# Optimization experiments

Hardware: AMD Instinct MI355X
Metric: run time of the kernel (lower is better)

## Reference

```python
import jax, jax.numpy as jnp
import numpy as np

N_NODES = 100000


def _gcn_conv(x, W, b, row, col, norm, n_nodes):
    # PyG GCNConv: h = x @ W; out[i] = sum_{(j->i)} norm_e * h[j] + b
    h = x @ W
    msg = h[row] * norm[:, None]              # [E_tot, out_dim] gather
    out = jax.ops.segment_sum(msg, col, num_segments=n_nodes)  # scatter-add
    return out + b


def _norm_and_loops(edge_index, n_nodes):
    # add self loops, compute symmetric normalization deg^-1/2 * deg^-1/2
    loop = jnp.arange(n_nodes, dtype=edge_index.dtype)
    row = jnp.concatenate([edge_index[0], loop])
    col = jnp.concatenate([edge_index[1], loop])
    deg = jax.ops.segment_sum(jnp.ones_like(col, dtype=jnp.float32), col,
                              num_segments=n_nodes)
    dis = jnp.where(deg > 0, jax.lax.rsqrt(jnp.maximum(deg, 1.0)), 0.0)
    norm = dis[row] * dis[col]
    return row, col, norm


def setup_inputs() -> dict:
    key = jax.random.key(0)
    ks = jax.random.split(key, 9)
    in_c, hid, lat = 128, 128, 64
    n_edges = 1600000
    x = jax.random.normal(ks[0], (N_NODES, in_c), dtype=jnp.float32)
    edge_index = jax.random.randint(ks[1], (2, n_edges), 0, N_NODES, dtype=jnp.int64)
    s1 = 1.0 / np.sqrt(in_c)
    s2 = 1.0 / np.sqrt(hid)
    W1 = jax.random.uniform(ks[2], (in_c, hid), jnp.float32, -s1, s1)
    b1 = jnp.zeros((hid,), jnp.float32)
    W_mu = jax.random.uniform(ks[3], (hid, lat), jnp.float32, -s2, s2)
    b_mu = jnp.zeros((lat,), jnp.float32)
    W_lv = jax.random.uniform(ks[4], (hid, lat), jnp.float32, -s2, s2)
    b_lv = jnp.zeros((lat,), jnp.float32)
    eps = jax.random.normal(ks[5], (N_NODES, lat), dtype=jnp.float32)
    return {"x": x, "edge_index": edge_index, "W1": W1, "b1": b1,
            "W_mu": W_mu, "b_mu": b_mu, "W_lv": W_lv, "b_lv": b_lv,
            "eps": eps}


def reference(x, edge_index, W1, b1, W_mu, b_mu, W_lv, b_lv, eps):
    row, col, norm = _norm_and_loops(edge_index, N_NODES)
    h = jax.nn.relu(_gcn_conv(x, W1, b1, row, col, norm, N_NODES))
    mu = _gcn_conv(h, W_mu, b_mu, row, col, norm, N_NODES)
    logvar = _gcn_conv(h, W_lv, b_lv, row, col, norm, N_NODES)
    # reparameterize (training mode): z = mu + eps * exp(0.5*logvar)
    z = mu + eps * jnp.exp(0.5 * logvar)
    return (z, mu, logvar)
```

## Files before the change

kernel.cpp:

```cpp
#include <hip/hip_runtime.h>
#include <math.h>


#define SHIFT 9
#define EPB 2048
#define HEPB 8192
#define CAP 15104

using f32x4 = __attribute__((ext_vector_type(4))) float;
using f16x8 = __attribute__((ext_vector_type(8))) _Float16;
using f16x2 = __attribute__((ext_vector_type(2))) _Float16;

__device__ inline int scan256(int v, int* wsum) {
    __syncthreads();
    int lane = threadIdx.x & 63, wid = threadIdx.x >> 6;
    int s = v;
#pragma unroll
    for (int d = 1; d < 64; d <<= 1) {
        int u = __shfl_up(s, d, 64);
        if (lane >= d) s += u;
    }
    if (lane == 63) wsum[wid] = s;
    __syncthreads();
    int off = 0;
    for (int w = 0; w < wid; w++) off += wsum[w];
    return off + s - v;
}

__global__ __launch_bounds__(256) void k_bhist(const int* __restrict__ coli,
                                               int* __restrict__ gbh,
                                               int E, int NB) {
    __shared__ int lh[4][256];
    int t = threadIdx.x, w = t >> 6;
    lh[0][t] = 0; lh[1][t] = 0; lh[2][t] = 0; lh[3][t] = 0;
    __syncthreads();
    int base = blockIdx.x * HEPB;
    for (int i = t; i < HEPB; i += 256) {
        int e = base + i;
        if (e < E) atomicAdd(&lh[w][coli[e] >> SHIFT], 1);
    }
    __syncthreads();
    if (t < NB) {
        int v = lh[0][t] + lh[1][t] + lh[2][t] + lh[3][t];
        if (v) atomicAdd(&gbh[t], v);
    }
}

__global__ __launch_bounds__(256) void k_bscan(const int* __restrict__ gbh,
                                               int* __restrict__ bptr,
                                               int* __restrict__ bcur,
                                               int NB, int E,
                                               int* __restrict__ rowptr, int N) {
    __shared__ int wsum[4];
    int t = threadIdx.x;
    int v = (t < NB) ? gbh[t] : 0;
    int e = scan256(v, wsum);
    if (t < NB) { bptr[t] = e; bcur[t] = e; }
    if (t == 0) { bptr[NB] = E; rowptr[N] = E; }
}

__global__ __launch_bounds__(256) void k_bucket(const int* __restrict__ rowi,
                                                const int* __restrict__ coli,
                                                int* __restrict__ bcur,
                                                int2* __restrict__ recs,
                                                int E, int NB) {
    __shared__ int lh[4][256], lcur[4][256], excl[256], gbase[256], wsum[4];
    __shared__ int2 stage[EPB];
    int t = threadIdx.x, w = t >> 6;
    lh[0][t] = 0; lh[1][t] = 0; lh[2][t] = 0; lh[3][t] = 0;
    __syncthreads();
    int base = blockIdx.x * EPB;
    int nE = min(EPB, E - base);
    for (int i = t; i < nE; i += 256)
        atomicAdd(&lh[w][coli[base + i] >> SHIFT], 1);
    __syncthreads();
    int h0 = lh[0][t], h1 = lh[1][t], h2 = lh[2][t], h3 = lh[3][t];
    int tot = h0 + h1 + h2 + h3;
    int ex = scan256(tot, wsum);
    excl[t] = ex;
    lcur[0][t] = ex;
    lcur[1][t] = ex + h0;
    lcur[2][t] = ex + h0 + h1;
    lcur[3][t] = ex + h0 + h1 + h2;
    if (t < NB && tot) gbase[t] = atomicAdd(&bcur[t], tot);
    __syncthreads();
    for (int i = t; i < nE; i += 256) {
        int r = rowi[base + i], c = coli[base + i];
        int p = atomicAdd(&lcur[w][c >> SHIFT], 1);
        stage[p] = make_int2(r, c);
    }
    __syncthreads();
    for (int i = t; i < nE; i += 256) {
        int2 r = stage[i];
        int bb = r.y >> SHIFT;
        recs[gbase[bb] + (i - excl[bb])] = r;
    }
}

__global__ __launch_bounds__(256) void k_fill2(const int2* __restrict__ recs,
                                               const int* __restrict__ bptr,
                                               int* __restrict__ rowptr,
                                               float* __restrict__ dis,
                                               int* __restrict__ srcs, int N) {
    __shared__ int hist[512], excl[512], wsum[4];
    __shared__ int srcsL[CAP];
    int t = threadIdx.x;
    int b = blockIdx.x;
    int nbase = b << SHIFT;
    int start = bptr[b], end = bptr[b + 1];
    int cnt = end - start;
    hist[t] = 0;
    hist[t + 256] = 0;
    __syncthreads();
    for (int i = start + t; i < end; i += 256)
        atomicAdd(&hist[recs[i].y - nbase], 1);
    __syncthreads();
    int h0 = hist[2 * t], h1 = hist[2 * t + 1];
    int e0 = scan256(h0 + h1, wsum);
    excl[2 * t] = e0;
    excl[2 * t + 1] = e0 + h0;
    int n0 = nbase + 2 * t, n1 = nbase + 2 * t + 1;
    if (n0 < N) { rowptr[n0] = start + e0;      dis[n0] = rsqrtf((float)(h0 + 1)); }
    if (n1 < N) { rowptr[n1] = start + e0 + h0; dis[n1] = rsqrtf((float)(h1 + 1)); }
    __syncthreads();
    if (cnt <= CAP) {
        for (int i = start + t; i < end; i += 256) {
            int2 r = recs[i];
            int p = atomicAdd(&excl[r.y - nbase], 1);
            srcsL[p] = r.x;
        }
        __syncthreads();
        for (int i = t; i < cnt; i += 256) srcs[start + i] = srcsL[i];
    } else {
        for (int i = start + t; i < end; i += 256) {
            int2 r = recs[i];
            int p = atomicAdd(&excl[r.y - nbase], 1);
            srcs[start + p] = r.x;
        }
    }
}

template <bool XF16>
__global__ __launch_bounds__(256) void k_gemm(const void* __restrict__ Xv,
                                              const float* __restrict__ Wa,
                                              const float* __restrict__ Wb,
                                              int split,
                                              const float* __restrict__ dis,
                                              _Float16* __restrict__ Y,
                                              int M, int ngroups) {
    __shared__ _Float16 Wl[16384];
    int tid = threadIdx.x;
    int wbs = 128 - split;
    for (int i = tid; i < 16384; i += 256) {
        int k = i >> 7, n = i & 127;
        float v = (n < split) ? Wa[k * split + n] : Wb[k * wbs + (n - split)];
        int tt = n >> 4, c = (k >> 5), q = (k >> 3) & 3, ln = q * 16 + (n & 15);
        Wl[(((tt * 4 + c) * 64) + ln) * 8 + (k & 7)] = (_Float16)v;
    }
    __syncthreads();

    int lane = tid & 63, w = tid >> 6;
    f16x8 B[32];
#pragma unroll
    for (int i = 0; i < 32; i++)
        B[i] = *(const f16x8*)&Wl[(i * 64 + lane) * 8];

    int m16 = lane & 15, quad = lane >> 4;
    for (int g = blockIdx.x; g < ngroups; g += gridDim.x) {
        int rowbase = g * 64 + w * 16;
        if (rowbase >= M) continue;
        int arow = min(rowbase + m16, M - 1);
        f16x8 A[4];
        if (XF16) {
            const _Float16* X = (const _Float16*)Xv;
#pragma unroll
            for (int c = 0; c < 4; c++)
                A[c] = *(const f16x8*)&X[arow * 128 + c * 32 + quad * 8];
        } else {
            const float* X = (const float*)Xv;
#pragma unroll
            for (int c = 0; c < 4; c++) {
                float4 u0 = *(const float4*)&X[arow * 128 + c * 32 + quad * 8];
                float4 u1 = *(const float4*)&X[arow * 128 + c * 32 + quad * 8 + 4];
                f16x8 a;
                a[0] = (_Float16)u0.x; a[1] = (_Float16)u0.y;
                a[2] = (_Float16)u0.z; a[3] = (_Float16)u0.w;
                a[4] = (_Float16)u1.x; a[5] = (_Float16)u1.y;
                a[6] = (_Float16)u1.z; a[7] = (_Float16)u1.w;
                A[c] = a;
            }
        }

        f32x4 acc[8];
#pragma unroll
        for (int t = 0; t < 8; t++) acc[t] = (f32x4)(0.f);
#pragma unroll
        for (int t = 0; t < 8; t++)
#pragma unroll
            for (int c = 0; c < 4; c++)
                acc[t] = __builtin_amdgcn_mfma_f32_16x16x32_f16(
                    A[c], B[t * 4 + c], acc[t], 0, 0, 0);

#pragma unroll
        for (int r = 0; r < 4; r++) {
            int row = rowbase + quad * 4 + r;
            if (row < M) {
                float d = dis[row];
#pragma unroll
                for (int t = 0; t < 8; t++)
                    Y[row * 128 + t * 16 + m16] = (_Float16)(d * acc[t][r]);
            }
        }
    }
}

template <bool OF16>
__global__ __launch_bounds__(256) void k_agg(const _Float16* __restrict__ F,
                                             const float* __restrict__ dis,
                                             const int* __restrict__ rowptr,
                                             const int* __restrict__ srcs,
                                             const float* __restrict__ ba,
                                             const float* __restrict__ bb,
                                             void* __restrict__ outA,
                                             void* __restrict__ outB,
                                             const float* __restrict__ eps,
                                             float* __restrict__ z, int N) {
    int node = blockIdx.x * 4 + (threadIdx.x >> 6);
    if (node >= N) return;
    int lane = threadIdx.x & 63;
    int g = lane >> 4, sl = lane & 15;
    const f16x8* Fr = (const f16x8*)F;

    float acc[8];
#pragma unroll
    for (int j = 0; j < 8; j++) acc[j] = 0.f;
    if (g == 0) {
        f16x8 v = Fr[node * 16 + sl];
#pragma unroll
        for (int j = 0; j < 8; j++) acc[j] = (float)v[j];
    }

    int s = rowptr[node], e = rowptr[node + 1];
    int t = s;
    for (; t + 8 <= e; t += 8) {
        int i0 = srcs[t + g];
        int i1 = srcs[t + 4 + g];
        f16x8 v0 = Fr[i0 * 16 + sl];
        f16x8 v1 = Fr[i1 * 16 + sl];
#pragma unroll
        for (int j = 0; j < 8; j++)
            acc[j] += (float)v0[j] + (float)v1[j];
    }
    if (t + 4 <= e) {
        int i0 = srcs[t + g];
        f16x8 v0 = Fr[i0 * 16 + sl];
#pragma unroll
        for (int j = 0; j < 8; j++) acc[j] += (float)v0[j];
        t += 4;
    }
    if (t < e) {
        int idx = t + g;
        bool ok = idx < e;
        int i0 = ok ? srcs[idx] : 0;
        f16x8 v0 = Fr[i0 * 16 + sl];
        if (ok) {
#pragma unroll
            for (int j = 0; j < 8; j++) acc[j] += (float)v0[j];
        }
    }

#pragma unroll
    for (int j = 0; j < 8; j++) {
        acc[j] += __shfl_xor(acc[j], 16);
        acc[j] += __shfl_xor(acc[j], 32);
    }

    float di = dis[node];
    if constexpr (OF16) {
        float4 b0 = *(const float4*)&ba[sl * 8];
        float4 b1 = *(const float4*)&ba[sl * 8 + 4];
        if (lane < 16) {
            f16x8 o;
            o[0] = (_Float16)fmaxf(fmaf(di, acc[0], b0.x), 0.f);
            o[1] = (_Float16)fmaxf(fmaf(di, acc[1], b0.y), 0.f);
            o[2] = (_Float16)fmaxf(fmaf(di, acc[2], b0.z), 0.f);
            o[3] = (_Float16)fmaxf(fmaf(di, acc[3], b0.w), 0.f);
            o[4] = (_Float16)fmaxf(fmaf(di, acc[4], b1.x), 0.f);
            o[5] = (_Float16)fmaxf(fmaf(di, acc[5], b1.y), 0.f);
            o[6] = (_Float16)fmaxf(fmaf(di, acc[6], b1.z), 0.f);
            o[7] = (_Float16)fmaxf(fmaf(di, acc[7], b1.w), 0.f);
            ((f16x8*)outA)[node * 16 + sl] = o;
        }
    } else {
        const float* bp = (sl < 8) ? ba : bb;
        int cb = (sl & 7) * 8;
        float4 b0 = *(const float4*)&bp[cb];
        float4 b1 = *(const float4*)&bp[cb + 4];
        float o[8];
        o[0] = fmaf(di, acc[0], b0.x);
        o[1] = fmaf(di, acc[1], b0.y);
        o[2] = fmaf(di, acc[2], b0.z);
        o[3] = fmaf(di, acc[3], b0.w);
        o[4] = fmaf(di, acc[4], b1.x);
        o[5] = fmaf(di, acc[5], b1.y);
        o[6] = fmaf(di, acc[6], b1.z);
        o[7] = fmaf(di, acc[7], b1.w);
        if (lane < 16) {
            float* op = (sl < 8) ? (float*)outA : (float*)outB;
            f32x4 s0, s1;
            s0[0] = o[0]; s0[1] = o[1]; s0[2] = o[2]; s0[3] = o[3];
            s1[0] = o[4]; s1[1] = o[5]; s1[2] = o[6]; s1[3] = o[7];
            __builtin_nontemporal_store(s0, (f32x4*)&op[node * 64 + cb]);
            __builtin_nontemporal_store(s1, (f32x4*)&op[node * 64 + cb + 4]);
        }
        float lvv[8];
#pragma unroll
        for (int j = 0; j < 8; j++) lvv[j] = __shfl_xor(o[j], 8);
        if (lane < 8) {
            int zb = node * 64 + sl * 8;
            float4 e0 = *(const float4*)&eps[zb];
            float4 e1 = *(const float4*)&eps[zb + 4];
            f32x4 z0, z1;
            z0[0] = fmaf(e0.x, expf(0.5f * lvv[0]), o[0]);
            z0[1] = fmaf(e0.y, expf(0.5f * lvv[1]), o[1]);
            z0[2] = fmaf(e0.z, expf(0.5f * lvv[2]), o[2]);
            z0[3] = fmaf(e0.w, expf(0.5f * lvv[3]), o[3]);
            z1[0] = fmaf(e1.x, expf(0.5f * lvv[4]), o[4]);
            z1[1] = fmaf(e1.y, expf(0.5f * lvv[5]), o[5]);
            z1[2] = fmaf(e1.z, expf(0.5f * lvv[6]), o[6]);
            z1[3] = fmaf(e1.w, expf(0.5f * lvv[7]), o[7]);
            __builtin_nontemporal_store(z0, (f32x4*)&z[zb]);
            __builtin_nontemporal_store(z1, (f32x4*)&z[zb + 4]);
        }
    }
}

extern "C" void kernel_launch(void* const* d_in, const int* in_sizes, int n_in,
                              void* d_out, int out_size, void* d_ws, size_t ws_size,
                              hipStream_t stream) {
    const float* x   = (const float*)d_in[0];
    const int*   ei  = (const int*)d_in[1];
    const float* W1  = (const float*)d_in[2];
    const float* b1  = (const float*)d_in[3];
    const float* Wmu = (const float*)d_in[4];
    const float* bmu = (const float*)d_in[5];
    const float* Wlv = (const float*)d_in[6];
    const float* blv = (const float*)d_in[7];
    const float* eps = (const float*)d_in[8];

    int N = in_sizes[0] / 128;
    int E = in_sizes[1] / 2;
    const int* rowi = ei;
    const int* coli = ei + E;
    int NB = (N + (1 << SHIFT) - 1) >> SHIFT;

    char* ws = (char*)d_ws;
    size_t off = 0;
    auto alloc = [&](size_t bytes) -> void* {
        void* p = ws + off;
        off += (bytes + 255) & ~(size_t)255;
        return p;
    };
    _Float16* bufA = (_Float16*)alloc((size_t)N * 128 * 2);
    _Float16* bufB = (_Float16*)alloc((size_t)N * 128 * 2);
    float* dis    = (float*)alloc((size_t)N * 4);
    int*   rowptr = (int*)alloc((size_t)(N + 1) * 4);
    int*   srcs   = (int*)alloc((size_t)E * 4);
    int2*  recs   = (int2*)alloc((size_t)E * 8);
    int*   bhist  = (int*)alloc((size_t)NB * 4);
    int*   bptr   = (int*)alloc((size_t)(NB + 1) * 4);
    int*   bcur   = (int*)alloc((size_t)NB * 4);

    float* zo  = (float*)d_out;
    float* muo = zo + (size_t)N * 64;
    float* lvo = zo + (size_t)N * 128;

    hipMemsetAsync(bhist, 0, (size_t)NB * 4, stream);
    k_bhist<<<(E + HEPB - 1) / HEPB, 256, 0, stream>>>(coli, bhist, E, NB);
    k_bscan<<<1, 256, 0, stream>>>(bhist, bptr, bcur, NB, E, rowptr, N);
    k_bucket<<<(E + EPB - 1) / EPB, 256, 0, stream>>>(rowi, coli, bcur, recs, E, NB);
    k_fill2<<<NB, 256, 0, stream>>>(recs, bptr, rowptr, dis, srcs, N);

    int ngroups = (N + 63) / 64;
    int gblk = ngroups < 640 ? ngroups : 640;
    k_gemm<false><<<gblk, 256, 0, stream>>>(x, W1, W1, 128, dis, bufA, N, ngroups);
    k_agg<true><<<(N + 3) / 4, 256, 0, stream>>>(bufA, dis, rowptr, srcs,
                                                 b1, b1, bufB, bufB,
                                                 nullptr, nullptr, N);
    k_gemm<true><<<gblk, 256, 0, stream>>>(bufB, Wmu, Wlv, 64, dis, bufA, N, ngroups);
    k_agg<false><<<(N + 3) / 4, 256, 0, stream>>>(bufA, dis, rowptr, srcs,
                                                  bmu, blv, muo, lvo,
                                                  eps, zo, N);
}
```

Measured before the change: 409.9 us.

## Segment CSR by source range and sweep segments in lockstep for cache locality

The fill kernel now sorts each destination node's neighbours into 13 source-index segments of 8192 nodes and writes per-node segment offsets (nsp) in place of a plain rowptr. The aggregation kernel gives each wave 13 consecutive destination nodes and walks source segments in order. The aim is that concurrently running waves gather from a similar slice of the feature matrix, so those gathers hit in L2 instead of going to HBM. In exchange, each lane now loads only f16x2 per gather instead of f16x8, and each wave works through longer serial per-node loops with more accumulator registers.

```diff
diff --git a/kernel.cpp b/kernel.cpp
--- a/kernel.cpp
+++ b/kernel.cpp
@@ -5,9 +5,15 @@
 #define SHIFT 9
 #define EPB 2048
 #define HEPB 8192
-#define CAP 15104
+
+#define SEG_SHIFT 13
+#define NSEG 13
+#define NSP_STRIDE 16
+#define KNODES 13
+#define AGG_BLOCKS 2048
 
 using f32x4 = __attribute__((ext_vector_type(4))) float;
+using f32x2 = __attribute__((ext_vector_type(2))) float;
 using f16x8 = __attribute__((ext_vector_type(8))) _Float16;
 using f16x2 = __attribute__((ext_vector_type(2))) _Float16;
 
@@ -49,14 +55,13 @@
 __global__ __launch_bounds__(256) void k_bscan(const int* __restrict__ gbh,
                                                int* __restrict__ bptr,
                                                int* __restrict__ bcur,
-                                               int NB, int E,
-                                               int* __restrict__ rowptr, int N) {
+                                               int NB, int E) {
     __shared__ int wsum[4];
     int t = threadIdx.x;
     int v = (t < NB) ? gbh[t] : 0;
     int e = scan256(v, wsum);
     if (t < NB) { bptr[t] = e; bcur[t] = e; }
-    if (t == 0) { bptr[NB] = E; rowptr[N] = E; }
+    if (t == 0) bptr[NB] = E;
 }
 
 __global__ __launch_bounds__(256) void k_bucket(const int* __restrict__ rowi,
@@ -99,44 +104,54 @@
 
 __global__ __launch_bounds__(256) void k_fill2(const int2* __restrict__ recs,
                                                const int* __restrict__ bptr,
-                                               int* __restrict__ rowptr,
+                                               int* __restrict__ nsp,
                                                float* __restrict__ dis,
                                                int* __restrict__ srcs, int N) {
-    __shared__ int hist[512], excl[512], wsum[4];
-    __shared__ int srcsL[CAP];
+    __shared__ int hist[512 * NSEG];
+    __shared__ int excl[512 * NSEG];
+    __shared__ int wsum[4];
     int t = threadIdx.x;
     int b = blockIdx.x;
     int nbase = b << SHIFT;
     int start = bptr[b], end = bptr[b + 1];
-    int cnt = end - start;
-    hist[t] = 0;
-    hist[t + 256] = 0;
-    __syncthreads();
-    for (int i = start + t; i < end; i += 256)
-        atomicAdd(&hist[recs[i].y - nbase], 1);
-    __syncthreads();
-    int h0 = hist[2 * t], h1 = hist[2 * t + 1];
-    int e0 = scan256(h0 + h1, wsum);
-    excl[2 * t] = e0;
-    excl[2 * t + 1] = e0 + h0;
-    int n0 = nbase + 2 * t, n1 = nbase + 2 * t + 1;
-    if (n0 < N) { rowptr[n0] = start + e0;      dis[n0] = rsqrtf((float)(h0 + 1)); }
-    if (n1 < N) { rowptr[n1] = start + e0 + h0; dis[n1] = rsqrtf((float)(h1 + 1)); }
-    __syncthreads();
-    if (cnt <= CAP) {
-        for (int i = start + t; i < end; i += 256) {
-            int2 r = recs[i];
-            int p = atomicAdd(&excl[r.y - nbase], 1);
-            srcsL[p] = r.x;
-        }
-        __syncthreads();
-        for (int i = t; i < cnt; i += 256) srcs[start + i] = srcsL[i];
-    } else {
-        for (int i = start + t; i < end; i += 256) {
-            int2 r = recs[i];
-            int p = atomicAdd(&excl[r.y - nbase], 1);
-            srcs[start + p] = r.x;
-        }
+    for (int i = t; i < 512 * NSEG; i += 256) hist[i] = 0;
+    __syncthreads();
+    for (int i = start + t; i < end; i += 256) {
+        int2 r = recs[i];
+        atomicAdd(&hist[(r.y - nbase) * NSEG + (r.x >> SEG_SHIFT)], 1);
+    }
+    __syncthreads();
+    int n0 = 2 * t, n1 = 2 * t + 1;
+    int tot0 = 0, tot1 = 0;
+#pragma unroll
+    for (int s = 0; s < NSEG; s++) {
+        tot0 += hist[n0 * NSEG + s];
+        tot1 += hist[n1 * NSEG + s];
+    }
+    int e0 = scan256(tot0 + tot1, wsum);
+    int g0 = nbase + n0, g1 = nbase + n1;
+    if (g0 < N) dis[g0] = rsqrtf((float)(tot0 + 1));
+    if (g1 < N) dis[g1] = rsqrtf((float)(tot1 + 1));
+    int c = start + e0;
+#pragma unroll
+    for (int s = 0; s < NSEG; s++) {
+        if (g0 < N) nsp[g0 * NSP_STRIDE + s] = c;
+        excl[n0 * NSEG + s] = c;
+        c += hist[n0 * NSEG + s];
+    }
+    if (g0 < N) nsp[g0 * NSP_STRIDE + NSEG] = c;
+#pragma unroll
+    for (int s = 0; s < NSEG; s++) {
+        if (g1 < N) nsp[g1 * NSP_STRIDE + s] = c;
+        excl[n1 * NSEG + s] = c;
+        c += hist[n1 * NSEG + s];
+    }
+    if (g1 < N) nsp[g1 * NSP_STRIDE + NSEG] = c;
+    __syncthreads();
+    for (int i = start + t; i < end; i += 256) {
+        int2 r = recs[i];
+        int p = atomicAdd(&excl[(r.y - nbase) * NSEG + (r.x >> SEG_SHIFT)], 1);
+        srcs[p] = r.x;
     }
 }
 
@@ -217,7 +232,7 @@
 template <bool OF16>
 __global__ __launch_bounds__(256) void k_agg(const _Float16* __restrict__ F,
                                              const float* __restrict__ dis,
-                                             const int* __restrict__ rowptr,
+                                             const int* __restrict__ nsp,
                                              const int* __restrict__ srcs,
                                              const float* __restrict__ ba,
                                              const float* __restrict__ bb,
@@ -225,112 +240,88 @@
                                              void* __restrict__ outB,
                                              const float* __restrict__ eps,
                                              float* __restrict__ z, int N) {
-    int node = blockIdx.x * 4 + (threadIdx.x >> 6);
-    if (node >= N) return;
+    int wv = blockIdx.x * 4 + (threadIdx.x >> 6);
     int lane = threadIdx.x & 63;
-    int g = lane >> 4, sl = lane & 15;
-    const f16x8* Fr = (const f16x8*)F;
-
-    float acc[8];
-#pragma unroll
-    for (int j = 0; j < 8; j++) acc[j] = 0.f;
-    if (g == 0) {
-        f16x8 v = Fr[node * 16 + sl];
-#pragma unroll
-        for (int j = 0; j < 8; j++) acc[j] = (float)v[j];
-    }
-
-    int s = rowptr[node], e = rowptr[node + 1];
-    int t = s;
-    for (; t + 8 <= e; t += 8) {
-        int i0 = srcs[t + g];
-        int i1 = srcs[t + 4 + g];
-        f16x8 v0 = Fr[i0 * 16 + sl];
-        f16x8 v1 = Fr[i1 * 16 + sl];
-#pragma unroll
-        for (int j = 0; j < 8; j++)
-            acc[j] += (float)v0[j] + (float)v1[j];
-    }
-    if (t + 4 <= e) {
-        int i0 = srcs[t + g];
-        f16x8 v0 = Fr[i0 * 16 + sl];
-#pragma unroll
-        for (int j = 0; j < 8; j++) acc[j] += (float)v0[j];
-        t += 4;
-    }
-    if (t < e) {
-        int idx = t + g;
-        bool ok = idx < e;
-        int i0 = ok ? srcs[idx] : 0;
-        f16x8 v0 = Fr[i0 * 16 + sl];
-        if (ok) {
-#pragma unroll
-            for (int j = 0; j < 8; j++) acc[j] += (float)v0[j];
-        }
-    }
-
-#pragma unroll
-    for (int j = 0; j < 8; j++) {
-        acc[j] += __shfl_xor(acc[j], 16);
-        acc[j] += __shfl_xor(acc[j], 32);
-    }
-
-    float di = dis[node];
+    int base = wv * KNODES;
+    const f16x2* Fv = (const f16x2*)F;
+
+    float ax[KNODES], ay[KNODES];
+    int cur[KNODES];
+#pragma unroll
+    for (int n = 0; n < KNODES; n++) {
+        ax[n] = 0.f;
+        ay[n] = 0.f;
+        int node = base + n;
+        cur[n] = (node < N) ? nsp[node * NSP_STRIDE] : 0;
+    }
+
+#pragma unroll 1
+    for (int s = 0; s < NSEG; s++) {
+#pragma unroll
+        for (int n = 0; n < KNODES; n++) {
+            int node = base + n;
+            if (node >= N) continue;
+            int nxt = nsp[node * NSP_STRIDE + s + 1];
+            if ((node >> SEG_SHIFT) == s) {
+                f16x2 v = Fv[node * 64 + lane];
+                ax[n] += (float)v[0];
+                ay[n] += (float)v[1];
+            }
+            int t = cur[n];
+            for (; t + 2 <= nxt; t += 2) {
+                int s0 = srcs[t], s1 = srcs[t + 1];
+                f16x2 v0 = Fv[s0 * 64 + lane];
+                f16x2 v1 = Fv[s1 * 64 + lane];
+                ax[n] += (float)v0[0] + (float)v1[0];
+                ay[n] += (float)v0[1] + (float)v1[1];
+            }
+            if (t < nxt) {
+                int s0 = srcs[t];
+                f16x2 v0 = Fv[s0 * 64 + lane];
+                ax[n] += (float)v0[0];
+                ay[n] += (float)v0[1];
+            }
+            cur[n] = nxt;
+        }
+    }
+
     if constexpr (OF16) {
-        float4 b0 = *(const float4*)&ba[sl * 8];
-        float4 b1 = *(const float4*)&ba[sl * 8 + 4];
-        if (lane < 16) {
-            f16x8 o;
-            o[0] = (_Float16)fmaxf(fmaf(di, acc[0], b0.x), 0.f);
-            o[1] = (_Float16)fmaxf(fmaf(di, acc[1], b0.y), 0.f);
-            o[2] = (_Float16)fmaxf(fmaf(di, acc[2], b0.z), 0.f);
-            o[3] = (_Float16)fmaxf(fmaf(di, acc[3], b0.w), 0.f);
-            o[4] = (_Float16)fmaxf(fmaf(di, acc[4], b1.x), 0.f);
-            o[5] = (_Float16)fmaxf(fmaf(di, acc[5], b1.y), 0.f);
-            o[6] = (_Float16)fmaxf(fmaf(di, acc[6], b1.z), 0.f);
-            o[7] = (_Float16)fmaxf(fmaf(di, acc[7], b1.w), 0.f);
-            ((f16x8*)outA)[node * 16 + sl] = o;
+        float bx = ba[2 * lane], by = ba[2 * lane + 1];
+#pragma unroll
+        for (int n = 0; n < KNODES; n++) {
+            int node = base + n;
+            if (node >= N) continue;
+            float di = dis[node];
+            f16x2 o;
+            o[0] = (_Float16)fmaxf(fmaf(di, ax[n], bx), 0.f);
+            o[1] = (_Float16)fmaxf(fmaf(di, ay[n], by), 0.f);
+            ((f16x2*)outA)[node * 64 + lane] = o;
         }
     } else {
-        const float* bp = (sl < 8) ? ba : bb;
-        int cb = (sl & 7) * 8;
-        float4 b0 = *(const float4*)&bp[cb];
-        float4 b1 = *(const float4*)&bp[cb + 4];
-        float o[8];
-        o[0] = fmaf(di, acc[0], b0.x);
-        o[1] = fmaf(di, acc[1], b0.y);
-        o[2] = fmaf(di, acc[2], b0.z);
-        o[3] = fmaf(di, acc[3], b0.w);
-        o[4] = fmaf(di, acc[4], b1.x);
-        o[5] = fmaf(di, acc[5], b1.y);
-        o[6] = fmaf(di, acc[6], b1.z);
-        o[7] = fmaf(di, acc[7], b1.w);
-        if (lane < 16) {
-            float* op = (sl < 8) ? (float*)outA : (float*)outB;
-            f32x4 s0, s1;
-            s0[0] = o[0]; s0[1] = o[1]; s0[2] = o[2]; s0[3] = o[3];
-            s1[0] = o[4]; s1[1] = o[5]; s1[2] = o[6]; s1[3] = o[7];
-            __builtin_nontemporal_store(s0, (f32x4*)&op[node * 64 + cb]);
-            __builtin_nontemporal_store(s1, (f32x4*)&op[node * 64 + cb + 4]);
-        }
-        float lvv[8];
-#pragma unroll
-        for (int j = 0; j < 8; j++) lvv[j] = __shfl_xor(o[j], 8);
-        if (lane < 8) {
-            int zb = node * 64 + sl * 8;
-            float4 e0 = *(const float4*)&eps[zb];
-            float4 e1 = *(const float4*)&eps[zb + 4];
-            f32x4 z0, z1;
-            z0[0] = fmaf(e0.x, expf(0.5f * lvv[0]), o[0]);
-            z0[1] = fmaf(e0.y, expf(0.5f * lvv[1]), o[1]);
-            z0[2] = fmaf(e0.z, expf(0.5f * lvv[2]), o[2]);
-            z0[3] = fmaf(e0.w, expf(0.5f * lvv[3]), o[3]);
-            z1[0] = fmaf(e1.x, expf(0.5f * lvv[4]), o[4]);
-            z1[1] = fmaf(e1.y, expf(0.5f * lvv[5]), o[5]);
-            z1[2] = fmaf(e1.z, expf(0.5f * lvv[6]), o[6]);
-            z1[3] = fmaf(e1.w, expf(0.5f * lvv[7]), o[7]);
-            __builtin_nontemporal_store(z0, (f32x4*)&z[zb]);
-            __builtin_nontemporal_store(z1, (f32x4*)&z[zb + 4]);
+        bool isMu = lane < 32;
+        int cb = isMu ? 2 * lane : 2 * lane - 64;
+        const float* bp = isMu ? ba : bb;
+        float bx = bp[cb], by = bp[cb + 1];
+        float* op = isMu ? (float*)outA : (float*)outB;
+#pragma unroll
+        for (int n = 0; n < KNODES; n++) {
+            int node = base + n;
+            if (node >= N) continue;
+            float di = dis[node];
+            float ox = fmaf(di, ax[n], bx);
+            float oy = fmaf(di, ay[n], by);
+            f32x2 ov;
+            ov[0] = ox; ov[1] = oy;
+            __builtin_nontemporal_store(ov, (f32x2*)&op[node * 64 + cb]);
+            float lx = __shfl_xor(ox, 32);
+            float ly = __shfl_xor(oy, 32);
+            if (isMu) {
+                float2 e = *(const float2*)&eps[node * 64 + cb];
+                f32x2 zv;
+                zv[0] = fmaf(e.x, expf(0.5f * lx), ox);
+                zv[1] = fmaf(e.y, expf(0.5f * ly), oy);
+                __builtin_nontemporal_store(zv, (f32x2*)&z[node * 64 + cb]);
+            }
         }
     }
 }
@@ -364,7 +355,7 @@
     _Float16* bufA = (_Float16*)alloc((size_t)N * 128 * 2);
     _Float16* bufB = (_Float16*)alloc((size_t)N * 128 * 2);
     float* dis    = (float*)alloc((size_t)N * 4);
-    int*   rowptr = (int*)alloc((size_t)(N + 1) * 4);
+    int*   nsp    = (int*)alloc((size_t)N * NSP_STRIDE * 4);
     int*   srcs   = (int*)alloc((size_t)E * 4);
     int2*  recs   = (int2*)alloc((size_t)E * 8);
     int*   bhist  = (int*)alloc((size_t)NB * 4);
@@ -377,18 +368,18 @@
 
     hipMemsetAsync(bhist, 0, (size_t)NB * 4, stream);
     k_bhist<<<(E + HEPB - 1) / HEPB, 256, 0, stream>>>(coli, bhist, E, NB);
-    k_bscan<<<1, 256, 0, stream>>>(bhist, bptr, bcur, NB, E, rowptr, N);
+    k_bscan<<<1, 256, 0, stream>>>(bhist, bptr, bcur, NB, E);
     k_bucket<<<(E + EPB - 1) / EPB, 256, 0, stream>>>(rowi, coli, bcur, recs, E, NB);
-    k_fill2<<<NB, 256, 0, stream>>>(recs, bptr, rowptr, dis, srcs, N);
+    k_fill2<<<NB, 256, 0, stream>>>(recs, bptr, nsp, dis, srcs, N);
 
     int ngroups = (N + 63) / 64;
     int gblk = ngroups < 640 ? ngroups : 640;
     k_gemm<false><<<gblk, 256, 0, stream>>>(x, W1, W1, 128, dis, bufA, N, ngroups);
-    k_agg<true><<<(N + 3) / 4, 256, 0, stream>>>(bufA, dis, rowptr, srcs,
-                                                 b1, b1, bufB, bufB,
-                                                 nullptr, nullptr, N);
+    k_agg<true><<<AGG_BLOCKS, 256, 0, stream>>>(bufA, dis, nsp, srcs,
+                                                b1, b1, bufB, bufB,
+                                                nullptr, nullptr, N);
     k_gemm<true><<<gblk, 256, 0, stream>>>(bufB, Wmu, Wlv, 64, dis, bufA, N, ngroups);
-    k_agg<false><<<(N + 3) / 4, 256, 0, stream>>>(bufA, dis, rowptr, srcs,
-                                                  bmu, blv, muo, lvo,
-                                                  eps, zo, N);
-}
+    k_agg<false><<<AGG_BLOCKS, 256, 0, stream>>>(bufA, dis, nsp, srcs,
+                                                 bmu, blv, muo, lvo,
+                                                 eps, zo, N);
+}
```

New measurement: 980.3 us. +139.2%, slower.
